# Kernel optimization log

Hardware: AMD Instinct MI355X
Metric: run time of the kernel (lower is better)

## Reference

```python
import jax, jax.numpy as jnp
import numpy as np

B, T, D = 64, 512, 1024
VOCAB = 50257


def setup_inputs() -> dict:
    key = jax.random.key(0)
    k1, k2, k3, k4 = jax.random.split(key, 4)
    vector_sequence = jax.random.normal(k1, (B, T, D), dtype=jnp.float32)
    # lengths in [1, T] to avoid degenerate all-zero rows (divide-by-zero, as in torch)
    sentence_length = jax.random.randint(k2, (B,), 1, T + 1, dtype=jnp.int32)
    word_sequence = jax.random.randint(k3, (B, T), 0, VOCAB, dtype=jnp.int32)
    # original init: 0.1 - 0.2*U[0,1) -> uniform in (-0.1, 0.1]
    weights = 0.1 - 0.2 * jax.random.uniform(k4, (VOCAB,), dtype=jnp.float32)
    return {
        "vector_sequence": vector_sequence,
        "sentence_length": sentence_length,
        "word_sequence": word_sequence,
        "weights": weights,
    }


def reference(vector_sequence, sentence_length, word_sequence, weights):
    # mask positions >= sentence_length (in-place zeroing in the original)
    mask = (jnp.arange(T)[None, :] < sentence_length[:, None]).astype(vector_sequence.dtype)  # [B,T]
    vs = vector_sequence * mask[:, :, None]  # [B,T,D]
    s = jnp.sum(vs, axis=1)  # [B,D]
    y = s / jnp.sqrt(jnp.sum(jnp.abs(s), axis=1, keepdims=True))  # [B,D]
    # per-token scalar weight gather, scale, masked sum over T
    w = weights[word_sequence] * mask  # [B,T]
    y_hat = jnp.einsum('btd,bt->bd', vs, w)  # [B,D]
    return (y, y_hat)
```

## Files before the change

kernel.cpp:

```cpp
#include <hip/hip_runtime.h>
#include <math.h>

constexpr int B = 64;
constexpr int T = 512;
constexpr int D = 1024;
constexpr int NT = 16;
constexpr int CHUNK = T / NT;

__global__ __launch_bounds__(256) void k1_partial(
    const float* __restrict__ vs,
    const int*   __restrict__ slen,
    const int*   __restrict__ words,
    const float* __restrict__ wts,
    float*       __restrict__ out)
{
    const int bid = blockIdx.x;
    const int b  = bid & (B - 1);
    const int tc = bid >> 6;
    const int len = slen[b];
    const int t0 = tc * CHUNK;
    if (t0 >= len) return;
    const int t1 = (t0 + CHUNK < len) ? (t0 + CHUNK) : len;

    __shared__ float wbuf[CHUNK];
    const int tid = threadIdx.x;
    if (tid < CHUNK) {
        const int t = t0 + tid;
        wbuf[tid] = (t < len) ? wts[words[b * T + t]] : 0.0f;
    }
    __syncthreads();

    const int d0 = tid * 4;
    const float4* vp = (const float4*)(vs + ((size_t)(b * T + t0)) * D + d0);
    float4 s  = make_float4(0.f, 0.f, 0.f, 0.f);
    float4 yh = make_float4(0.f, 0.f, 0.f, 0.f);

    for (int t = t0; t < t1; ++t) {
        const float4 v = *vp;
        vp += D / 4;
        const float w = wbuf[t - t0];
        s.x += v.x; s.y += v.y; s.z += v.z; s.w += v.w;
        yh.x += v.x * w; yh.y += v.y * w; yh.z += v.z * w; yh.w += v.w * w;
    }

    float* so = out + (size_t)b * D + d0;
    float* yo = out + (size_t)(B + b) * D + d0;
    atomicAdd(so + 0, s.x);  atomicAdd(so + 1, s.y);
    atomicAdd(so + 2, s.z);  atomicAdd(so + 3, s.w);
    atomicAdd(yo + 0, yh.x); atomicAdd(yo + 1, yh.y);
    atomicAdd(yo + 2, yh.z); atomicAdd(yo + 3, yh.w);
}

__global__ __launch_bounds__(256) void k2_normalize(float* __restrict__ out)
{
    const int b = blockIdx.x;
    const int tid = threadIdx.x;
    float* sp = out + (size_t)b * D + tid * 4;
    const float4 s = *(const float4*)sp;

    float a = fabsf(s.x) + fabsf(s.y) + fabsf(s.z) + fabsf(s.w);
    for (int off = 32; off > 0; off >>= 1)
        a += __shfl_down(a, off, 64);

    __shared__ float part[4];
    const int wave = tid >> 6;
    const int lane = tid & 63;
    if (lane == 0) part[wave] = a;
    __syncthreads();
    const float tot = part[0] + part[1] + part[2] + part[3];
    const float inv = 1.0f / sqrtf(tot);

    float4 y;
    y.x = s.x * inv; y.y = s.y * inv; y.z = s.z * inv; y.w = s.w * inv;
    *(float4*)sp = y;
}

extern "C" void kernel_launch(void* const* d_in, const int* in_sizes, int n_in,
                              void* d_out, int out_size, void* d_ws, size_t ws_size,
                              hipStream_t stream) {
    const float* vs    = (const float*)d_in[0];
    const int*   slen  = (const int*)  d_in[1];
    const int*   words = (const int*)  d_in[2];
    const float* wts   = (const float*)d_in[3];
    float* out = (float*)d_out;

    hipMemsetAsync(out, 0, (size_t)2 * B * D * sizeof(float), stream);

    k1_partial<<<B * NT, 256, 0, stream>>>(vs, slen, words, wts, out);
    k2_normalize<<<B, 256, 0, stream>>>(out);
}
```

Measured before the change: 199.0 us.

## Replace atomic accumulation with workspace partials reduced in finalize kernel

```diff
diff --git a/kernel.cpp b/kernel.cpp
--- a/kernel.cpp
+++ b/kernel.cpp
@@ -7,12 +7,13 @@
 constexpr int NT = 16;
 constexpr int CHUNK = T / NT;
 
+
 __global__ __launch_bounds__(256) void k1_partial(
     const float* __restrict__ vs,
     const int*   __restrict__ slen,
     const int*   __restrict__ words,
     const float* __restrict__ wts,
-    float*       __restrict__ out)
+    float*       __restrict__ part)
 {
     const int bid = blockIdx.x;
     const int b  = bid & (B - 1);
@@ -35,6 +36,7 @@
     float4 s  = make_float4(0.f, 0.f, 0.f, 0.f);
     float4 yh = make_float4(0.f, 0.f, 0.f, 0.f);
 
+    #pragma unroll 4
     for (int t = t0; t < t1; ++t) {
         const float4 v = *vp;
         vp += D / 4;
@@ -43,36 +45,48 @@
         yh.x += v.x * w; yh.y += v.y * w; yh.z += v.z * w; yh.w += v.w * w;
     }
 
-    float* so = out + (size_t)b * D + d0;
-    float* yo = out + (size_t)(B + b) * D + d0;
-    atomicAdd(so + 0, s.x);  atomicAdd(so + 1, s.y);
-    atomicAdd(so + 2, s.z);  atomicAdd(so + 3, s.w);
-    atomicAdd(yo + 0, yh.x); atomicAdd(yo + 1, yh.y);
-    atomicAdd(yo + 2, yh.z); atomicAdd(yo + 3, yh.w);
+    float* p = part + ((size_t)tc * B + b) * (2 * D) + d0;
+    *(float4*)p       = s;
+    *(float4*)(p + D) = yh;
 }
 
-__global__ __launch_bounds__(256) void k2_normalize(float* __restrict__ out)
+__global__ __launch_bounds__(256) void k2_finalize(
+    const float* __restrict__ part,
+    const int*   __restrict__ slen,
+    float*       __restrict__ out)
 {
     const int b = blockIdx.x;
     const int tid = threadIdx.x;
-    float* sp = out + (size_t)b * D + tid * 4;
-    const float4 s = *(const float4*)sp;
+    const int len = slen[b];
+    const int nact = (len + CHUNK - 1) / CHUNK;
+
+    const int d0 = tid * 4;
+    float4 s  = make_float4(0.f, 0.f, 0.f, 0.f);
+    float4 yh = make_float4(0.f, 0.f, 0.f, 0.f);
+    for (int tc = 0; tc < nact; ++tc) {
+        const float* p = part + ((size_t)tc * B + b) * (2 * D) + d0;
+        const float4 ps = *(const float4*)p;
+        const float4 py = *(const float4*)(p + D);
+        s.x += ps.x; s.y += ps.y; s.z += ps.z; s.w += ps.w;
+        yh.x += py.x; yh.y += py.y; yh.z += py.z; yh.w += py.w;
+    }
 
     float a = fabsf(s.x) + fabsf(s.y) + fabsf(s.z) + fabsf(s.w);
     for (int off = 32; off > 0; off >>= 1)
         a += __shfl_down(a, off, 64);
 
-    __shared__ float part[4];
+    __shared__ float psum[4];
     const int wave = tid >> 6;
     const int lane = tid & 63;
-    if (lane == 0) part[wave] = a;
+    if (lane == 0) psum[wave] = a;
     __syncthreads();
-    const float tot = part[0] + part[1] + part[2] + part[3];
+    const float tot = psum[0] + psum[1] + psum[2] + psum[3];
     const float inv = 1.0f / sqrtf(tot);
 
     float4 y;
     y.x = s.x * inv; y.y = s.y * inv; y.z = s.z * inv; y.w = s.w * inv;
-    *(float4*)sp = y;
+    *(float4*)(out + (size_t)b * D + d0)       = y;
+    *(float4*)(out + (size_t)(B + b) * D + d0) = yh;
 }
 
 extern "C" void kernel_launch(void* const* d_in, const int* in_sizes, int n_in,
@@ -82,10 +96,9 @@
     const int*   slen  = (const int*)  d_in[1];
     const int*   words = (const int*)  d_in[2];
     const float* wts   = (const float*)d_in[3];
-    float* out = (float*)d_out;
+    float* out  = (float*)d_out;
+    float* part = (float*)d_ws;
 
-    hipMemsetAsync(out, 0, (size_t)2 * B * D * sizeof(float), stream);
-
-    k1_partial<<<B * NT, 256, 0, stream>>>(vs, slen, words, wts, out);
-    k2_normalize<<<B, 256, 0, stream>>>(out);
+    k1_partial <<<B * NT, 256, 0, stream>>>(vs, slen, words, wts, part);
+    k2_finalize<<<B,      256, 0, stream>>>(part, slen, out);
 }
```

Result: faster. 186.9 us (-6.1%).
